# Kernel optimization log

Hardware: AMD Instinct MI355X
Metric: run time of the kernel (lower is better)

Reference implementation:

```python
import jax, jax.numpy as jnp
import numpy as np

T, B, D, H = 1024, 64, 512, 512


def setup_inputs() -> dict:
    key = jax.random.key(0)
    ks = jax.random.split(key, 10)
    s_in = 1.0 / np.sqrt(D + H)  # torch Linear default init scale
    inp = {
        "inputs": jax.random.normal(ks[0], (T, B, D), dtype=jnp.float32),
        "Wf": jax.random.uniform(ks[1], (D + H, H), jnp.float32, -s_in, s_in),
        "bf": jax.random.uniform(ks[2], (H,), jnp.float32, -s_in, s_in),
        "Wi": jax.random.uniform(ks[3], (D + H, H), jnp.float32, -s_in, s_in),
        "bi": jax.random.uniform(ks[4], (H,), jnp.float32, -s_in, s_in),
        "Wg": jax.random.uniform(ks[5], (D + H, H), jnp.float32, -s_in, s_in),
        "bg": jax.random.uniform(ks[6], (H,), jnp.float32, -s_in, s_in),
        "Wo": jax.random.uniform(ks[7], (D + H, H), jnp.float32, -s_in, s_in),
        "bo": jax.random.uniform(ks[8], (H,), jnp.float32, -s_in, s_in),
        "phase_bias": jax.random.normal(ks[9], (H,), dtype=jnp.float32) * 0.02,
    }
    return inp


def reference(inputs, Wf, bf, Wi, bi, Wg, bg, Wo, bo, phase_bias):
    gate_scale = 1.0
    Bsz = inputs.shape[1]
    Hd = Wf.shape[1]
    # Fuse the four gate projections into one GEMM per step (same math).
    W = jnp.concatenate([Wf, Wi, Wg, Wo], axis=1)          # [D+H, 4H]
    bias = jnp.concatenate([bf, bi, bg, bo]) * gate_scale + jnp.tile(phase_bias, 4)
    # note: (x@W + b)*s + pb == x@(W*s) + (b*s + pb); gate_scale folded in.
    Ws = W * gate_scale

    h0 = jnp.zeros((Bsz, Hd), dtype=inputs.dtype)
    c0 = jnp.zeros((Bsz, Hd), dtype=inputs.dtype)

    def step(carry, x):
        hx, cx = carry
        combined = jnp.concatenate([x, hx], axis=1)         # [B, D+H]
        z = combined @ Ws + bias                            # [B, 4H]
        zf, zi, zg, zo = jnp.split(z, 4, axis=1)
        f = jax.nn.sigmoid(zf)
        i = jax.nn.sigmoid(zi)
        g = jnp.tanh(zg)
        o = jax.nn.sigmoid(zo)
        cx = f * cx + i * g
        hx = o * jnp.tanh(cx)
        return (hx, cx), hx

    (hx, cx), stacked = jax.lax.scan(step, (h0, c0), inputs)
    return stacked, hx, cx
```

## Files before the change

kernel.cpp:

```cpp
#include <hip/hip_runtime.h>

#define TT 1024
#define BB 64
#define DD 512
#define HH 512
#define NG 4
#define BPG 16
#define NS 32
#define UPS 16
#define NTHR 256

typedef short s8v __attribute__((ext_vector_type(8)));
typedef float f4v __attribute__((ext_vector_type(4)));
typedef int i4v __attribute__((ext_vector_type(4)));

#define ASWZ(row, kbyte) ((((row) * 2048) + (kbyte)) ^ (((row) & 7) << 4))

static __device__ __forceinline__ unsigned short f2bf(float f) {
  union { float f; unsigned int u; } v; v.f = f;
  unsigned int r = v.u + 0x7FFFu + ((v.u >> 16) & 1u);
  return (unsigned short)(r >> 16);
}

static __device__ __forceinline__ i4v ld_b128_cohere(const void* p) {
  i4v r;
  asm volatile("global_load_dwordx4 %0, %1, off sc0 sc1"
               : "=v"(r) : "v"(p) : "memory");
  return r;
}
static __device__ __forceinline__ int ld_b32_cohere(const void* p) {
  int r;
  asm volatile("global_load_dword %0, %1, off sc0 sc1\n\t"
               "s_waitcnt vmcnt(0)"
               : "=v"(r) : "v"(p) : "memory");
  return r;
}
static __device__ __forceinline__ void st_b32_cohere(void* p, unsigned int v) {
  asm volatile("global_store_dword %0, %1, off sc0 sc1"
               :: "v"(p), "v"(v) : "memory");
}
static __device__ __forceinline__ unsigned int cvtpk_bf16(float lo, float hi) {
  unsigned int r;
  asm("v_cvt_pk_bf16_f32 %0, %1, %2" : "=v"(r) : "v"(lo), "v"(hi));
  return r;
}

__global__ void __launch_bounds__(256, 1) qlstm_init(int* flags) {
  st_b32_cohere(flags + threadIdx.x, 0u);
}

struct SMem {
  char ab[16 * 1024 * 2];
  float zp[4][64][17];
};

__global__ void __launch_bounds__(NTHR, 1) qlstm_main(
    const float* __restrict__ X,
    const float* __restrict__ Wf, const float* __restrict__ bfp,
    const float* __restrict__ Wi, const float* __restrict__ bip,
    const float* __restrict__ Wg, const float* __restrict__ bgp,
    const float* __restrict__ Wo, const float* __restrict__ bop,
    const float* __restrict__ phase,
    float* __restrict__ out, int* __restrict__ flags,
    unsigned short* __restrict__ hbuf) {
  __shared__ SMem sm;
  const int tid  = threadIdx.x;
  const int wv   = tid >> 6;
  const int lane = tid & 63;
  const int group = blockIdx.x & (NG - 1);
  const int slice = blockIdx.x / NG;
  const int b0 = group * BPG;
  const int u0 = slice * UPS;
  const int gb = tid >> 4;
  const int gu = tid & 15;

  const float* Wm[4] = {Wf, Wi, Wg, Wo};
  const int ucol  = u0 + (lane & 15);
  const int krow0 = wv * 256 + ((lane >> 4) << 3);
  s8v wreg[8][4];
#pragma unroll
  for (int kk = 0; kk < 8; ++kk) {
#pragma unroll
    for (int cf = 0; cf < 4; ++cf) {
      const float* Wp = Wm[cf] + (size_t)(krow0 + kk * 32) * HH + ucol;
      s8v w;
#pragma unroll
      for (int j = 0; j < 8; ++j) w[j] = (short)f2bf(Wp[(size_t)j * HH]);
      wreg[kk][cf] = w;
    }
  }

  const int uu = u0 + gu;
  float breg[4] = {bfp[uu] + phase[uu], bip[uu] + phase[uu],
                   bgp[uu] + phase[uu], bop[uu] + phase[uu]};
  float creg = 0.f;

  {
    const float4* Xr = (const float4*)(X + ((size_t)0 * BB + b0 + gb) * DD);
    float4 xv[8];
#pragma unroll
    for (int j = 0; j < 8; ++j) xv[j] = Xr[gu + 16 * j];
#pragma unroll
    for (int j = 0; j < 8; ++j) {
      uint2 pk;
      pk.x = cvtpk_bf16(xv[j].x, xv[j].y);
      pk.y = cvtpk_bf16(xv[j].z, xv[j].w);
      *(uint2*)(sm.ab + ASWZ(gb, (4 * gu + 64 * j) * 2)) = pk;
    }
  }
  __syncthreads();

  const int arow = lane & 15;
  int* myflag = flags + group * 64 + slice;
  const int* pollp = flags + group * 64 + (lane & 31);

  for (int t = 0; t < TT; ++t) {
    f4v acc[4] = {{0.f, 0.f, 0.f, 0.f}, {0.f, 0.f, 0.f, 0.f},
                  {0.f, 0.f, 0.f, 0.f}, {0.f, 0.f, 0.f, 0.f}};
    if (wv < 2 || t > 0) {
      if (wv >= 2) {
        for (;;) {
          const int v = ld_b32_cohere(pollp);
          if (__all(v >= t)) break;
          __builtin_amdgcn_s_sleep(1);
        }
        const int urow  = lane & 15;
        const int ucol0 = (wv - 2) * 256 + ((lane >> 4) << 6);
        const unsigned short* hb =
            hbuf + (size_t)((t - 1) & 1) * BB * HH + (b0 + urow) * HH + ucol0;
        i4v hr[8];
#pragma unroll
        for (int j = 0; j < 8; ++j) hr[j] = ld_b128_cohere(hb + j * 8);
        asm volatile("s_waitcnt vmcnt(0)" ::: "memory");
        __builtin_amdgcn_sched_barrier(0);
#pragma unroll
        for (int j = 0; j < 8; ++j)
          *(i4v*)(sm.ab + ASWZ(urow, 1024 + (ucol0 + j * 8) * 2)) = hr[j];
      }
      const int kbyte0 = wv * 512 + ((lane >> 4) << 4);
#pragma unroll
      for (int kk = 0; kk < 8; ++kk) {
        const s8v af = *(const s8v*)(sm.ab + ASWZ(arow, kbyte0 + kk * 64));
#pragma unroll
        for (int cf = 0; cf < 4; ++cf)
          acc[cf] = __builtin_amdgcn_mfma_f32_16x16x32_bf16(af, wreg[kk][cf],
                                                            acc[cf], 0, 0, 0);
      }
    }
#pragma unroll
    for (int cf = 0; cf < 4; ++cf)
#pragma unroll
      for (int i = 0; i < 4; ++i)
        sm.zp[wv][cf * 16 + (lane & 15)][((lane >> 4) << 2) + i] = acc[cf][i];
    __syncthreads();

    float4 xv[8];
    const bool px = (t + 1 < TT);
    if (px) {
      const float4* Xr = (const float4*)(X + ((size_t)(t + 1) * BB + b0 + gb) * DD);
#pragma unroll
      for (int j = 0; j < 8; ++j) xv[j] = Xr[gu + 16 * j];
    }
    float z[4];
#pragma unroll
    for (int cf = 0; cf < 4; ++cf)
      z[cf] = sm.zp[0][cf * 16 + gu][gb] + sm.zp[1][cf * 16 + gu][gb] +
              sm.zp[2][cf * 16 + gu][gb] + sm.zp[3][cf * 16 + gu][gb] + breg[cf];
    const float fg = 1.f / (1.f + __expf(-z[0]));
    const float ig = 1.f / (1.f + __expf(-z[1]));
    const float gg = 1.f - 2.f / (__expf(2.f * z[2]) + 1.f);
    const float og = 1.f / (1.f + __expf(-z[3]));
    creg = fg * creg + ig * gg;
    const float hv = og * (1.f - 2.f / (__expf(2.f * creg) + 1.f));

    const float hn = __shfl_down(hv, 1);
    if (!(gu & 1)) {
      unsigned short* hp =
          hbuf + (size_t)(t & 1) * BB * HH + (b0 + gb) * HH + (u0 + gu);
      st_b32_cohere(hp, cvtpk_bf16(hv, hn));
    }
    out[(size_t)t * (BB * HH) + (b0 + gb) * HH + (u0 + gu)] = hv;
    if (t == TT - 1) {
      out[(size_t)TT * BB * HH + (b0 + gb) * HH + (u0 + gu)] = hv;
      out[(size_t)TT * BB * HH + BB * HH + (b0 + gb) * HH + (u0 + gu)] = creg;
    }
    if (px) {
#pragma unroll
      for (int j = 0; j < 8; ++j) {
        uint2 pk;
        pk.x = cvtpk_bf16(xv[j].x, xv[j].y);
        pk.y = cvtpk_bf16(xv[j].z, xv[j].w);
        *(uint2*)(sm.ab + ASWZ(gb, (4 * gu + 64 * j) * 2)) = pk;
      }
    }
    asm volatile("s_waitcnt vmcnt(0)" ::: "memory");
    __syncthreads();
    if (tid == 0) st_b32_cohere(myflag, (unsigned int)(t + 1));
  }
}

extern "C" void kernel_launch(void* const* d_in, const int* in_sizes, int n_in,
                              void* d_out, int out_size, void* d_ws,
                              size_t ws_size, hipStream_t stream) {
  const float* X   = (const float*)d_in[0];
  const float* Wf  = (const float*)d_in[1];
  const float* bfp = (const float*)d_in[2];
  const float* Wi  = (const float*)d_in[3];
  const float* bip = (const float*)d_in[4];
  const float* Wg  = (const float*)d_in[5];
  const float* bgp = (const float*)d_in[6];
  const float* Wo  = (const float*)d_in[7];
  const float* bop = (const float*)d_in[8];
  const float* ph  = (const float*)d_in[9];
  float* out = (float*)d_out;

  int* flags = (int*)d_ws;
  unsigned short* hbuf = (unsigned short*)((char*)d_ws + 8192);

  qlstm_init<<<1, 256, 0, stream>>>(flags);
  qlstm_main<<<NG * NS, NTHR, 0, stream>>>(X, Wf, bfp, Wi, bip, Wg, bgp, Wo,
                                           bop, ph, out, flags, hbuf);
}
```

Baseline: 3.466 ms.

## Split waves into input-projection producers and recurrent consumers with register-resident h operands

Waves 0-1 now compute the input projection x_t·W_x one timestep ahead into a double-buffered LDS array. Waves 2-3 do only the recurrent h·W_h GEMM, so that work overlaps the serial dependency chain instead of sitting on it. The recurrent waves load h straight from global memory into MFMA operand registers, which removes the LDS staging of h and the four-way LDS partial-sum reduction. Gate pairs are combined with a lane shuffle, and each h wave publishes its own completion flag. The cost is larger per-wave weight register footprints and more flag polling per step.

After: 4.602 ms. 1.33x slower.

```diff
diff --git a/kernel.cpp b/kernel.cpp
--- a/kernel.cpp
+++ b/kernel.cpp
@@ -14,8 +14,6 @@
 typedef float f4v __attribute__((ext_vector_type(4)));
 typedef int i4v __attribute__((ext_vector_type(4)));
 
-#define ASWZ(row, kbyte) ((((row) * 2048) + (kbyte)) ^ (((row) & 7) << 4))
-
 static __device__ __forceinline__ unsigned short f2bf(float f) {
   union { float f; unsigned int u; } v; v.f = f;
   unsigned int r = v.u + 0x7FFFu + ((v.u >> 16) & 1u);
@@ -49,10 +47,27 @@
   st_b32_cohere(flags + threadIdx.x, 0u);
 }
 
-struct SMem {
-  char ab[16 * 1024 * 2];
-  float zp[4][64][17];
-};
+static __device__ __forceinline__ void x_gemm(
+    const float* __restrict__ X, int t, int b0, int n, int kg,
+    const s8v* wreg0, const s8v* wreg1,
+    float* __restrict__ zdst0, float* __restrict__ zdst1) {
+  const float* Xb = X + ((size_t)t * BB + b0 + n) * DD + kg * 8;
+  f4v a0 = {0.f, 0.f, 0.f, 0.f}, a1 = {0.f, 0.f, 0.f, 0.f};
+#pragma unroll
+  for (int kc = 0; kc < 16; ++kc) {
+    const float4 xa = *(const float4*)(Xb + kc * 32);
+    const float4 xb = *(const float4*)(Xb + kc * 32 + 4);
+    union { s8v s; unsigned int d[4]; } af;
+    af.d[0] = cvtpk_bf16(xa.x, xa.y);
+    af.d[1] = cvtpk_bf16(xa.z, xa.w);
+    af.d[2] = cvtpk_bf16(xb.x, xb.y);
+    af.d[3] = cvtpk_bf16(xb.z, xb.w);
+    a0 = __builtin_amdgcn_mfma_f32_16x16x32_bf16(af.s, wreg0[kc], a0, 0, 0, 0);
+    a1 = __builtin_amdgcn_mfma_f32_16x16x32_bf16(af.s, wreg1[kc], a1, 0, 0, 0);
+  }
+#pragma unroll
+  for (int i = 0; i < 4; ++i) { zdst0[i * 64] = a0[i]; zdst1[i * 64] = a1[i]; }
+}
 
 __global__ void __launch_bounds__(NTHR, 1) qlstm_main(
     const float* __restrict__ X,
@@ -63,139 +78,135 @@
     const float* __restrict__ phase,
     float* __restrict__ out, int* __restrict__ flags,
     unsigned short* __restrict__ hbuf) {
-  __shared__ SMem sm;
-  const int tid  = threadIdx.x;
-  const int wv   = tid >> 6;
-  const int lane = tid & 63;
+  __shared__ float zpx[2][2][2][4][64];
+  const int tid   = threadIdx.x;
+  const int wv    = tid >> 6;
+  const int lane  = tid & 63;
+  const int n     = lane & 15;
+  const int kg    = lane >> 4;
   const int group = blockIdx.x & (NG - 1);
   const int slice = blockIdx.x / NG;
   const int b0 = group * BPG;
   const int u0 = slice * UPS;
-  const int gb = tid >> 4;
-  const int gu = tid & 15;
-
-  const float* Wm[4] = {Wf, Wi, Wg, Wo};
-  const int ucol  = u0 + (lane & 15);
-  const int krow0 = wv * 256 + ((lane >> 4) << 3);
-  s8v wreg[8][4];
-#pragma unroll
-  for (int kk = 0; kk < 8; ++kk) {
-#pragma unroll
-    for (int cf = 0; cf < 4; ++cf) {
-      const float* Wp = Wm[cf] + (size_t)(krow0 + kk * 32) * HH + ucol;
-      s8v w;
-#pragma unroll
-      for (int j = 0; j < 8; ++j) w[j] = (short)f2bf(Wp[(size_t)j * HH]);
-      wreg[kk][cf] = w;
+  const bool isH = (wv >= 2);
+  const int uh = wv & 1;
+
+  const float* Wt0 = (n < 8) ? Wf : Wi;
+  const float* Wt1 = (n < 8) ? Wg : Wo;
+  const int wcol  = u0 + uh * 8 + (n & 7);
+  const int krow0 = (isH ? 512 : 0) + kg * 8;
+  s8v wreg0[16], wreg1[16];
+#pragma unroll
+  for (int kc = 0; kc < 16; ++kc) {
+#pragma unroll
+    for (int j = 0; j < 8; ++j) {
+      const int row = krow0 + kc * 32 + j;
+      wreg0[kc][j] = (short)f2bf(Wt0[(size_t)row * HH + wcol]);
+      wreg1[kc][j] = (short)f2bf(Wt1[(size_t)row * HH + wcol]);
     }
   }
 
-  const int uu = u0 + gu;
-  float breg[4] = {bfp[uu] + phase[uu], bip[uu] + phase[uu],
-                   bgp[uu] + phase[uu], bop[uu] + phase[uu]};
-  float creg = 0.f;
-
-  {
-    const float4* Xr = (const float4*)(X + ((size_t)0 * BB + b0 + gb) * DD);
-    float4 xv[8];
-#pragma unroll
-    for (int j = 0; j < 8; ++j) xv[j] = Xr[gu + 16 * j];
-#pragma unroll
-    for (int j = 0; j < 8; ++j) {
-      uint2 pk;
-      pk.x = cvtpk_bf16(xv[j].x, xv[j].y);
-      pk.y = cvtpk_bf16(xv[j].z, xv[j].w);
-      *(uint2*)(sm.ab + ASWZ(gb, (4 * gu + 64 * j) * 2)) = pk;
+  if (!isH) {
+    x_gemm(X, 0, b0, n, kg, wreg0, wreg1,
+           &zpx[0][uh][0][0][lane], &zpx[0][uh][1][0][lane]);
+    __syncthreads();
+    for (int t = 0; t < TT; ++t) {
+      if (t + 1 < TT)
+        x_gemm(X, t + 1, b0, n, kg, wreg0, wreg1,
+               &zpx[(t + 1) & 1][uh][0][0][lane],
+               &zpx[(t + 1) & 1][uh][1][0][lane]);
+      asm volatile("s_waitcnt lgkmcnt(0)" ::: "memory");
+      __builtin_amdgcn_sched_barrier(0);
+      __builtin_amdgcn_s_barrier();
+      __builtin_amdgcn_sched_barrier(0);
     }
-  }
-  __syncthreads();
-
-  const int arow = lane & 15;
-  int* myflag = flags + group * 64 + slice;
-  const int* pollp = flags + group * 64 + (lane & 31);
-
-  for (int t = 0; t < TT; ++t) {
-    f4v acc[4] = {{0.f, 0.f, 0.f, 0.f}, {0.f, 0.f, 0.f, 0.f},
-                  {0.f, 0.f, 0.f, 0.f}, {0.f, 0.f, 0.f, 0.f}};
-    if (wv < 2 || t > 0) {
-      if (wv >= 2) {
+  } else {
+    const int uu = u0 + uh * 8 + (n & 7);
+    const float bz0 = bfp[uu] + phase[uu];
+    const float bz1 = bip[uu] + phase[uu];
+    const float bz2 = bgp[uu] + phase[uu];
+    const float bz3 = bop[uu] + phase[uu];
+    float cst[4] = {0.f, 0.f, 0.f, 0.f};
+    int* myflag = flags + (uh * NG + group) * NS + slice;
+    const int* pollp = flags + ((lane >> 5) * NG + group) * NS + (lane & 31);
+
+    __syncthreads();
+    for (int t = 0; t < TT; ++t) {
+      f4v px0, px1;
+#pragma unroll
+      for (int i = 0; i < 4; ++i) {
+        px0[i] = zpx[t & 1][uh][0][i][lane];
+        px1[i] = zpx[t & 1][uh][1][i][lane];
+      }
+      f4v a0 = {0.f, 0.f, 0.f, 0.f}, a1 = {0.f, 0.f, 0.f, 0.f};
+      if (t > 0) {
         for (;;) {
           const int v = ld_b32_cohere(pollp);
           if (__all(v >= t)) break;
           __builtin_amdgcn_s_sleep(1);
         }
-        const int urow  = lane & 15;
-        const int ucol0 = (wv - 2) * 256 + ((lane >> 4) << 6);
-        const unsigned short* hb =
-            hbuf + (size_t)((t - 1) & 1) * BB * HH + (b0 + urow) * HH + ucol0;
-        i4v hr[8];
-#pragma unroll
-        for (int j = 0; j < 8; ++j) hr[j] = ld_b128_cohere(hb + j * 8);
+        const unsigned short* hb = hbuf + (size_t)((t - 1) & 1) * BB * HH +
+                                   (size_t)(b0 + n) * HH + kg * 8;
+        i4v hf[16];
+#pragma unroll
+        for (int kc = 0; kc < 16; ++kc) hf[kc] = ld_b128_cohere(hb + kc * 32);
         asm volatile("s_waitcnt vmcnt(0)" ::: "memory");
         __builtin_amdgcn_sched_barrier(0);
 #pragma unroll
-        for (int j = 0; j < 8; ++j)
-          *(i4v*)(sm.ab + ASWZ(urow, 1024 + (ucol0 + j * 8) * 2)) = hr[j];
-      }
-      const int kbyte0 = wv * 512 + ((lane >> 4) << 4);
-#pragma unroll
-      for (int kk = 0; kk < 8; ++kk) {
-        const s8v af = *(const s8v*)(sm.ab + ASWZ(arow, kbyte0 + kk * 64));
-#pragma unroll
-        for (int cf = 0; cf < 4; ++cf)
-          acc[cf] = __builtin_amdgcn_mfma_f32_16x16x32_bf16(af, wreg[kk][cf],
-                                                            acc[cf], 0, 0, 0);
-      }
+        for (int kc = 0; kc < 16; ++kc) {
+          union { i4v i; s8v s; } af; af.i = hf[kc];
+          a0 = __builtin_amdgcn_mfma_f32_16x16x32_bf16(af.s, wreg0[kc], a0, 0, 0, 0);
+          a1 = __builtin_amdgcn_mfma_f32_16x16x32_bf16(af.s, wreg1[kc], a1, 0, 0, 0);
+        }
+      }
+      float hv[4];
+#pragma unroll
+      for (int i = 0; i < 4; ++i) {
+        const float s0 = a0[i] + px0[i];
+        const float s1 = a1[i] + px1[i];
+        const float p0 = __shfl_xor(s0, 8);
+        const float p1 = __shfl_xor(s1, 8);
+        const bool lo = (n < 8);
+        const float zf = (lo ? s0 : p0) + bz0;
+        const float zi = (lo ? p0 : s0) + bz1;
+        const float zg = (lo ? s1 : p1) + bz2;
+        const float zo = (lo ? p1 : s1) + bz3;
+        const float fg = 1.f / (1.f + __expf(-zf));
+        const float ig = 1.f / (1.f + __expf(-zi));
+        const float gg = 1.f - 2.f / (__expf(2.f * zg) + 1.f);
+        const float og = 1.f / (1.f + __expf(-zo));
+        cst[i] = fg * cst[i] + ig * gg;
+        hv[i] = og * (1.f - 2.f / (__expf(2.f * cst[i]) + 1.f));
+      }
+      float hn[4];
+#pragma unroll
+      for (int i = 0; i < 4; ++i) hn[i] = __shfl_down(hv[i], 1);
+      unsigned short* hp = hbuf + (size_t)(t & 1) * BB * HH;
+      if (n < 8 && !(n & 1)) {
+#pragma unroll
+        for (int i = 0; i < 4; ++i)
+          st_b32_cohere(hp + (size_t)(b0 + 4 * kg + i) * HH + (u0 + uh * 8 + n),
+                        cvtpk_bf16(hv[i], hn[i]));
+      }
+      asm volatile("s_waitcnt vmcnt(0)" ::: "memory");
+      if (lane == 0) st_b32_cohere(myflag, (unsigned int)(t + 1));
+      if (n < 8) {
+#pragma unroll
+        for (int i = 0; i < 4; ++i)
+          out[(size_t)t * BB * HH + (size_t)(b0 + 4 * kg + i) * HH + uu] = hv[i];
+        if (t == TT - 1) {
+#pragma unroll
+          for (int i = 0; i < 4; ++i) {
+            out[(size_t)TT * BB * HH + (size_t)(b0 + 4 * kg + i) * HH + uu] = hv[i];
+            out[(size_t)TT * BB * HH + BB * HH +
+                (size_t)(b0 + 4 * kg + i) * HH + uu] = cst[i];
+          }
+        }
+      }
+      __builtin_amdgcn_sched_barrier(0);
+      __builtin_amdgcn_s_barrier();
+      __builtin_amdgcn_sched_barrier(0);
     }
-#pragma unroll
-    for (int cf = 0; cf < 4; ++cf)
-#pragma unroll
-      for (int i = 0; i < 4; ++i)
-        sm.zp[wv][cf * 16 + (lane & 15)][((lane >> 4) << 2) + i] = acc[cf][i];
-    __syncthreads();
-
-    float4 xv[8];
-    const bool px = (t + 1 < TT);
-    if (px) {
-      const float4* Xr = (const float4*)(X + ((size_t)(t + 1) * BB + b0 + gb) * DD);
-#pragma unroll
-      for (int j = 0; j < 8; ++j) xv[j] = Xr[gu + 16 * j];
-    }
-    float z[4];
-#pragma unroll
-    for (int cf = 0; cf < 4; ++cf)
-      z[cf] = sm.zp[0][cf * 16 + gu][gb] + sm.zp[1][cf * 16 + gu][gb] +
-              sm.zp[2][cf * 16 + gu][gb] + sm.zp[3][cf * 16 + gu][gb] + breg[cf];
-    const float fg = 1.f / (1.f + __expf(-z[0]));
-    const float ig = 1.f / (1.f + __expf(-z[1]));
-    const float gg = 1.f - 2.f / (__expf(2.f * z[2]) + 1.f);
-    const float og = 1.f / (1.f + __expf(-z[3]));
-    creg = fg * creg + ig * gg;
-    const float hv = og * (1.f - 2.f / (__expf(2.f * creg) + 1.f));
-
-    const float hn = __shfl_down(hv, 1);
-    if (!(gu & 1)) {
-      unsigned short* hp =
-          hbuf + (size_t)(t & 1) * BB * HH + (b0 + gb) * HH + (u0 + gu);
-      st_b32_cohere(hp, cvtpk_bf16(hv, hn));
-    }
-    out[(size_t)t * (BB * HH) + (b0 + gb) * HH + (u0 + gu)] = hv;
-    if (t == TT - 1) {
-      out[(size_t)TT * BB * HH + (b0 + gb) * HH + (u0 + gu)] = hv;
-      out[(size_t)TT * BB * HH + BB * HH + (b0 + gb) * HH + (u0 + gu)] = creg;
-    }
-    if (px) {
-#pragma unroll
-      for (int j = 0; j < 8; ++j) {
-        uint2 pk;
-        pk.x = cvtpk_bf16(xv[j].x, xv[j].y);
-        pk.y = cvtpk_bf16(xv[j].z, xv[j].w);
-        *(uint2*)(sm.ab + ASWZ(gb, (4 * gu + 64 * j) * 2)) = pk;
-      }
-    }
-    asm volatile("s_waitcnt vmcnt(0)" ::: "memory");
-    __syncthreads();
-    if (tid == 0) st_b32_cohere(myflag, (unsigned int)(t + 1));
   }
 }
 
@@ -215,7 +226,7 @@
   float* out = (float*)d_out;
 
   int* flags = (int*)d_ws;
-  unsigned short* hbuf = (unsigned short*)((char*)d_ws + 8192);
+  unsigned short* hbuf = (unsigned short*)((char*)d_ws + 4096);
 
   qlstm_init<<<1, 256, 0, stream>>>(flags);
   qlstm_main<<<NG * NS, NTHR, 0, stream>>>(X, Wf, bfp, Wi, bip, Wg, bgp, Wo,
```

## Split x and h projections across waves and precompute next-step x gates

Applied to the files above, without the earlier changes.

Waves 0-1 now compute the input projection for step t+1 while waves 2-3 wait on the h flags and compute the recurrent projection for step t. A-operands come straight from registers instead of going through swizzled LDS, and the x loads for t+2 are prefetched. The output store moves after the flag publish, which shortens the per-step critical path. The cost is that only two waves do the h MFMAs on the serial path (each over 256 of K), and there are extra zx/zh LDS buffers with parity double-buffering.

After: 3.121 ms. -9.9%, faster.

```diff
diff --git a/kernel.cpp b/kernel.cpp
--- a/kernel.cpp
+++ b/kernel.cpp
@@ -7,21 +7,17 @@
 #define NG 4
 #define BPG 16
 #define NS 32
-#define UPS 16
 #define NTHR 256
 
 typedef short s8v __attribute__((ext_vector_type(8)));
 typedef float f4v __attribute__((ext_vector_type(4)));
 typedef int i4v __attribute__((ext_vector_type(4)));
-
-#define ASWZ(row, kbyte) ((((row) * 2048) + (kbyte)) ^ (((row) & 7) << 4))
 
 static __device__ __forceinline__ unsigned short f2bf(float f) {
   union { float f; unsigned int u; } v; v.f = f;
   unsigned int r = v.u + 0x7FFFu + ((v.u >> 16) & 1u);
   return (unsigned short)(r >> 16);
 }
-
 static __device__ __forceinline__ i4v ld_b128_cohere(const void* p) {
   i4v r;
   asm volatile("global_load_dwordx4 %0, %1, off sc0 sc1"
@@ -45,14 +41,9 @@
   return r;
 }
 
-__global__ void __launch_bounds__(256, 1) qlstm_init(int* flags) {
+__global__ void __launch_bounds__(128, 1) qlstm_init(int* flags) {
   st_b32_cohere(flags + threadIdx.x, 0u);
 }
-
-struct SMem {
-  char ab[16 * 1024 * 2];
-  float zp[4][64][17];
-};
 
 __global__ void __launch_bounds__(NTHR, 1) qlstm_main(
     const float* __restrict__ X,
@@ -63,139 +54,168 @@
     const float* __restrict__ phase,
     float* __restrict__ out, int* __restrict__ flags,
     unsigned short* __restrict__ hbuf) {
-  __shared__ SMem sm;
-  const int tid  = threadIdx.x;
-  const int wv   = tid >> 6;
-  const int lane = tid & 63;
+  __shared__ float zx[2][2][4][64][4];
+  __shared__ float zh[2][4][64][4];
+  const int tid   = threadIdx.x;
+  const int wv    = tid >> 6;
+  const int lane  = tid & 63;
+  const int n     = lane & 15;
+  const int kg    = lane >> 4;
   const int group = blockIdx.x & (NG - 1);
-  const int slice = blockIdx.x / NG;
+  const int slice = blockIdx.x >> 2;
   const int b0 = group * BPG;
-  const int u0 = slice * UPS;
-  const int gb = tid >> 4;
-  const int gu = tid & 15;
-
-  const float* Wm[4] = {Wf, Wi, Wg, Wo};
-  const int ucol  = u0 + (lane & 15);
-  const int krow0 = wv * 256 + ((lane >> 4) << 3);
-  s8v wreg[8][4];
-#pragma unroll
-  for (int kk = 0; kk < 8; ++kk) {
-#pragma unroll
-    for (int cf = 0; cf < 4; ++cf) {
-      const float* Wp = Wm[cf] + (size_t)(krow0 + kk * 32) * HH + ucol;
-      s8v w;
-#pragma unroll
-      for (int j = 0; j < 8; ++j) w[j] = (short)f2bf(Wp[(size_t)j * HH]);
-      wreg[kk][cf] = w;
-    }
+  const int u0 = slice * 16;
+  const bool isH = (wv >= 2);
+  const int kh = wv & 1;
+
+  const int wcol = u0 + (n & 7);
+  s8v wreg[4][8];
+#pragma unroll
+  for (int T = 0; T < 4; ++T) {
+    const float* Wsel = (T & 1) ? ((n < 8) ? Wg : Wo) : ((n < 8) ? Wf : Wi);
+    const float* Wp = Wsel + (size_t)((isH ? 512 : 0) + kh * 256 + kg * 8) * HH
+                    + wcol + (T >> 1) * 8;
+#pragma unroll
+    for (int kc = 0; kc < 8; ++kc)
+#pragma unroll
+      for (int j = 0; j < 8; ++j)
+        wreg[T][kc][j] = (short)f2bf(Wp[(size_t)(kc * 32 + j) * HH]);
   }
 
+  const int gb = tid >> 4, gu = tid & 15;
   const int uu = u0 + gu;
-  float breg[4] = {bfp[uu] + phase[uu], bip[uu] + phase[uu],
-                   bgp[uu] + phase[uu], bop[uu] + phase[uu]};
-  float creg = 0.f;
-
-  {
-    const float4* Xr = (const float4*)(X + ((size_t)0 * BB + b0 + gb) * DD);
-    float4 xv[8];
-#pragma unroll
-    for (int j = 0; j < 8; ++j) xv[j] = Xr[gu + 16 * j];
-#pragma unroll
-    for (int j = 0; j < 8; ++j) {
-      uint2 pk;
-      pk.x = cvtpk_bf16(xv[j].x, xv[j].y);
-      pk.y = cvtpk_bf16(xv[j].z, xv[j].w);
-      *(uint2*)(sm.ab + ASWZ(gb, (4 * gu + 64 * j) * 2)) = pk;
+  const float bzf = bfp[uu] + phase[uu];
+  const float bzi = bip[uu] + phase[uu];
+  const float bzg = bgp[uu] + phase[uu];
+  const float bzo = bop[uu] + phase[uu];
+  float cst = 0.f;
+
+  for (int p = tid; p < 2 * 4 * 64 * 4; p += NTHR) ((float*)zh)[p] = 0.f;
+  float4 xv[16];
+  s8v xf[8];
+  if (!isH) {
+    const float* Xr = X + ((size_t)0 * BB + b0 + n) * DD + kh * 256 + kg * 8;
+#pragma unroll
+    for (int kc = 0; kc < 8; ++kc) {
+      xv[2 * kc]     = *(const float4*)(Xr + kc * 32);
+      xv[2 * kc + 1] = *(const float4*)(Xr + kc * 32 + 4);
+    }
+#pragma unroll
+    for (int kc = 0; kc < 8; ++kc) {
+      union { s8v s; unsigned int d[4]; } af;
+      af.d[0] = cvtpk_bf16(xv[2 * kc].x, xv[2 * kc].y);
+      af.d[1] = cvtpk_bf16(xv[2 * kc].z, xv[2 * kc].w);
+      af.d[2] = cvtpk_bf16(xv[2 * kc + 1].x, xv[2 * kc + 1].y);
+      af.d[3] = cvtpk_bf16(xv[2 * kc + 1].z, xv[2 * kc + 1].w);
+      xf[kc] = af.s;
+    }
+    f4v acc[4] = {{0.f,0.f,0.f,0.f},{0.f,0.f,0.f,0.f},{0.f,0.f,0.f,0.f},{0.f,0.f,0.f,0.f}};
+#pragma unroll
+    for (int kc = 0; kc < 8; ++kc)
+#pragma unroll
+      for (int T = 0; T < 4; ++T)
+        acc[T] = __builtin_amdgcn_mfma_f32_16x16x32_bf16(xf[kc], wreg[T][kc], acc[T], 0, 0, 0);
+#pragma unroll
+    for (int T = 0; T < 4; ++T) *(f4v*)&zx[0][kh][T][lane][0] = acc[T];
+    const float* X1 = X + ((size_t)1 * BB + b0 + n) * DD + kh * 256 + kg * 8;
+#pragma unroll
+    for (int kc = 0; kc < 8; ++kc) {
+      xv[2 * kc]     = *(const float4*)(X1 + kc * 32);
+      xv[2 * kc + 1] = *(const float4*)(X1 + kc * 32 + 4);
     }
   }
-  __syncthreads();
-
-  const int arow = lane & 15;
-  int* myflag = flags + group * 64 + slice;
-  const int* pollp = flags + group * 64 + (lane & 31);
+
+  int* myflag = flags + group * NS + slice;
+  const int* pollp = flags + group * NS + (lane & 31);
 
   for (int t = 0; t < TT; ++t) {
-    f4v acc[4] = {{0.f, 0.f, 0.f, 0.f}, {0.f, 0.f, 0.f, 0.f},
-                  {0.f, 0.f, 0.f, 0.f}, {0.f, 0.f, 0.f, 0.f}};
-    if (wv < 2 || t > 0) {
-      if (wv >= 2) {
-        for (;;) {
-          const int v = ld_b32_cohere(pollp);
-          if (__all(v >= t)) break;
-          __builtin_amdgcn_s_sleep(1);
+    if (!isH) {
+      if (t + 1 < TT) {
+#pragma unroll
+        for (int kc = 0; kc < 8; ++kc) {
+          union { s8v s; unsigned int d[4]; } af;
+          af.d[0] = cvtpk_bf16(xv[2 * kc].x, xv[2 * kc].y);
+          af.d[1] = cvtpk_bf16(xv[2 * kc].z, xv[2 * kc].w);
+          af.d[2] = cvtpk_bf16(xv[2 * kc + 1].x, xv[2 * kc + 1].y);
+          af.d[3] = cvtpk_bf16(xv[2 * kc + 1].z, xv[2 * kc + 1].w);
+          xf[kc] = af.s;
         }
-        const int urow  = lane & 15;
-        const int ucol0 = (wv - 2) * 256 + ((lane >> 4) << 6);
-        const unsigned short* hb =
-            hbuf + (size_t)((t - 1) & 1) * BB * HH + (b0 + urow) * HH + ucol0;
-        i4v hr[8];
-#pragma unroll
-        for (int j = 0; j < 8; ++j) hr[j] = ld_b128_cohere(hb + j * 8);
-        asm volatile("s_waitcnt vmcnt(0)" ::: "memory");
-        __builtin_amdgcn_sched_barrier(0);
-#pragma unroll
-        for (int j = 0; j < 8; ++j)
-          *(i4v*)(sm.ab + ASWZ(urow, 1024 + (ucol0 + j * 8) * 2)) = hr[j];
-      }
-      const int kbyte0 = wv * 512 + ((lane >> 4) << 4);
-#pragma unroll
-      for (int kk = 0; kk < 8; ++kk) {
-        const s8v af = *(const s8v*)(sm.ab + ASWZ(arow, kbyte0 + kk * 64));
-#pragma unroll
-        for (int cf = 0; cf < 4; ++cf)
-          acc[cf] = __builtin_amdgcn_mfma_f32_16x16x32_bf16(af, wreg[kk][cf],
-                                                            acc[cf], 0, 0, 0);
-      }
-    }
-#pragma unroll
-    for (int cf = 0; cf < 4; ++cf)
-#pragma unroll
-      for (int i = 0; i < 4; ++i)
-        sm.zp[wv][cf * 16 + (lane & 15)][((lane >> 4) << 2) + i] = acc[cf][i];
+        f4v acc[4] = {{0.f,0.f,0.f,0.f},{0.f,0.f,0.f,0.f},{0.f,0.f,0.f,0.f},{0.f,0.f,0.f,0.f}};
+#pragma unroll
+        for (int kc = 0; kc < 8; ++kc)
+#pragma unroll
+          for (int T = 0; T < 4; ++T)
+            acc[T] = __builtin_amdgcn_mfma_f32_16x16x32_bf16(xf[kc], wreg[T][kc], acc[T], 0, 0, 0);
+#pragma unroll
+        for (int T = 0; T < 4; ++T)
+          *(f4v*)&zx[(t + 1) & 1][kh][T][lane][0] = acc[T];
+      }
+    } else if (t > 0) {
+      for (;;) {
+        const int v = ld_b32_cohere(pollp);
+        if (__all(v >= t)) break;
+        __builtin_amdgcn_s_sleep(1);
+      }
+      const unsigned short* hb = hbuf + (size_t)((t - 1) & 1) * BB * HH +
+                                 (size_t)(b0 + n) * HH + kh * 256 + kg * 8;
+      i4v hf[8];
+#pragma unroll
+      for (int kc = 0; kc < 8; ++kc) hf[kc] = ld_b128_cohere(hb + kc * 32);
+      asm volatile("s_waitcnt vmcnt(0)" ::: "memory");
+      __builtin_amdgcn_sched_barrier(0);
+      f4v acc[4] = {{0.f,0.f,0.f,0.f},{0.f,0.f,0.f,0.f},{0.f,0.f,0.f,0.f},{0.f,0.f,0.f,0.f}};
+#pragma unroll
+      for (int kc = 0; kc < 8; ++kc) {
+        union { i4v i; s8v s; } af; af.i = hf[kc];
+#pragma unroll
+        for (int T = 0; T < 4; ++T)
+          acc[T] = __builtin_amdgcn_mfma_f32_16x16x32_bf16(af.s, wreg[T][kc], acc[T], 0, 0, 0);
+      }
+#pragma unroll
+      for (int T = 0; T < 4; ++T) *(f4v*)&zh[kh][T][lane][0] = acc[T];
+    }
     __syncthreads();
 
-    float4 xv[8];
-    const bool px = (t + 1 < TT);
-    if (px) {
-      const float4* Xr = (const float4*)(X + ((size_t)(t + 1) * BB + b0 + gb) * DD);
-#pragma unroll
-      for (int j = 0; j < 8; ++j) xv[j] = Xr[gu + 16 * j];
-    }
-    float z[4];
-#pragma unroll
-    for (int cf = 0; cf < 4; ++cf)
-      z[cf] = sm.zp[0][cf * 16 + gu][gb] + sm.zp[1][cf * 16 + gu][gb] +
-              sm.zp[2][cf * 16 + gu][gb] + sm.zp[3][cf * 16 + gu][gb] + breg[cf];
-    const float fg = 1.f / (1.f + __expf(-z[0]));
-    const float ig = 1.f / (1.f + __expf(-z[1]));
-    const float gg = 1.f - 2.f / (__expf(2.f * z[2]) + 1.f);
-    const float og = 1.f / (1.f + __expf(-z[3]));
-    creg = fg * creg + ig * gg;
-    const float hv = og * (1.f - 2.f / (__expf(2.f * creg) + 1.f));
+    const int par = t & 1;
+    const int Lf  = (gb >> 2) * 16 + (gu & 7);
+    const int T0  = (gu >> 3) * 2;
+    const int ci  = gb & 3;
+    const float zfv = zx[par][0][T0][Lf][ci]     + zx[par][1][T0][Lf][ci]
+                    + zh[0][T0][Lf][ci]          + zh[1][T0][Lf][ci] + bzf;
+    const float ziv = zx[par][0][T0][Lf+8][ci]   + zx[par][1][T0][Lf+8][ci]
+                    + zh[0][T0][Lf+8][ci]        + zh[1][T0][Lf+8][ci] + bzi;
+    const float zgv = zx[par][0][T0+1][Lf][ci]   + zx[par][1][T0+1][Lf][ci]
+                    + zh[0][T0+1][Lf][ci]        + zh[1][T0+1][Lf][ci] + bzg;
+    const float zov = zx[par][0][T0+1][Lf+8][ci] + zx[par][1][T0+1][Lf+8][ci]
+                    + zh[0][T0+1][Lf+8][ci]      + zh[1][T0+1][Lf+8][ci] + bzo;
+    const float fg = 1.f / (1.f + __expf(-zfv));
+    const float ig = 1.f / (1.f + __expf(-ziv));
+    const float gg = 1.f - 2.f / (__expf(2.f * zgv) + 1.f);
+    const float og = 1.f / (1.f + __expf(-zov));
+    cst = fg * cst + ig * gg;
+    const float hv = og * (1.f - 2.f / (__expf(2.f * cst) + 1.f));
 
     const float hn = __shfl_down(hv, 1);
-    if (!(gu & 1)) {
-      unsigned short* hp =
-          hbuf + (size_t)(t & 1) * BB * HH + (b0 + gb) * HH + (u0 + gu);
-      st_b32_cohere(hp, cvtpk_bf16(hv, hn));
-    }
-    out[(size_t)t * (BB * HH) + (b0 + gb) * HH + (u0 + gu)] = hv;
-    if (t == TT - 1) {
-      out[(size_t)TT * BB * HH + (b0 + gb) * HH + (u0 + gu)] = hv;
-      out[(size_t)TT * BB * HH + BB * HH + (b0 + gb) * HH + (u0 + gu)] = creg;
-    }
-    if (px) {
-#pragma unroll
-      for (int j = 0; j < 8; ++j) {
-        uint2 pk;
-        pk.x = cvtpk_bf16(xv[j].x, xv[j].y);
-        pk.y = cvtpk_bf16(xv[j].z, xv[j].w);
-        *(uint2*)(sm.ab + ASWZ(gb, (4 * gu + 64 * j) * 2)) = pk;
-      }
-    }
+    if (!(gu & 1))
+      st_b32_cohere(hbuf + (size_t)par * BB * HH + (size_t)(b0 + gb) * HH + uu,
+                    cvtpk_bf16(hv, hn));
     asm volatile("s_waitcnt vmcnt(0)" ::: "memory");
+    if (!isH && t + 2 < TT) {
+      const float* Xr = X + ((size_t)(t + 2) * BB + b0 + n) * DD + kh * 256 + kg * 8;
+#pragma unroll
+      for (int kc = 0; kc < 8; ++kc) {
+        xv[2 * kc]     = *(const float4*)(Xr + kc * 32);
+        xv[2 * kc + 1] = *(const float4*)(Xr + kc * 32 + 4);
+      }
+    }
     __syncthreads();
     if (tid == 0) st_b32_cohere(myflag, (unsigned int)(t + 1));
+
+    out[(size_t)t * BB * HH + (size_t)(b0 + gb) * HH + uu] = hv;
+    if (t == TT - 1) {
+      out[(size_t)TT * BB * HH + (size_t)(b0 + gb) * HH + uu] = hv;
+      out[(size_t)TT * BB * HH + BB * HH + (size_t)(b0 + gb) * HH + uu] = cst;
+    }
   }
 }
 
@@ -215,9 +235,9 @@
   float* out = (float*)d_out;
 
   int* flags = (int*)d_ws;
-  unsigned short* hbuf = (unsigned short*)((char*)d_ws + 8192);
-
-  qlstm_init<<<1, 256, 0, stream>>>(flags);
+  unsigned short* hbuf = (unsigned short*)((char*)d_ws + 4096);
+
+  qlstm_init<<<1, 128, 0, stream>>>(flags);
   qlstm_main<<<NG * NS, NTHR, 0, stream>>>(X, Wf, bfp, Wi, bip, Wg, bgp, Wo,
                                            bop, ph, out, flags, hbuf);
 }
```
